# Kernel tuning notes

Measured on AMD Instinct MI355X. Metric: run time of the kernel, lower is better.

Reference implementation:

```python
import jax, jax.numpy as jnp
import numpy as np

EMBED = 2048
HEADS = 16
HEAD_DIM = EMBED // HEADS


def setup_inputs() -> dict:
    key = jax.random.key(0)
    k1, k2 = jax.random.split(key)
    X = jax.random.normal(k1, (2, 2048, EMBED), dtype=jnp.float32)
    W_qkv = jax.random.normal(k2, (EMBED, 3 * EMBED), dtype=jnp.float32) * (1.0 / np.sqrt(EMBED))
    b_qkv = jnp.zeros((3 * EMBED,), dtype=jnp.float32)
    return {"X": X, "W_qkv": W_qkv, "b_qkv": b_qkv}


def reference(X, W_qkv, b_qkv):
    B, S, D = X.shape
    qkv = jnp.einsum('bsd,de->bse', X, W_qkv) + b_qkv  # [B,S,3D]
    q, k, v = jnp.split(qkv, 3, axis=-1)
    # [B,S,D] -> [B,H,S,hd]
    def heads(t):
        return t.reshape(B, S, HEADS, HEAD_DIM).transpose(0, 2, 1, 3)
    q, k, v = heads(q), heads(k), heads(v)
    scale = 1.0 / np.sqrt(HEAD_DIM).astype(np.float32)
    attention_score = jnp.einsum('bhqd,bhkd->bhqk', q, k) * scale
    scores = jax.nn.softmax(attention_score, axis=-1)  # [B,H,S,S]
    attention = jnp.einsum('bhqk,bhkd->bhqd', scores, v)
    attention = attention.transpose(0, 2, 1, 3).reshape(B, S, D)
    return (attention, scores)
```

## Files before the change

### kernel.cpp

```cpp
#include <hip/hip_runtime.h>
#include <hip/hip_bf16.h>

typedef __attribute__((ext_vector_type(8))) short short8;
typedef __attribute__((ext_vector_type(4))) float floatx4;

#define SEQ 2048
#define EMB 2048
#define NH 16
#define HD 128
#define E3 6144

static __device__ __forceinline__ unsigned short f2bf(float f) {
  unsigned u = __builtin_bit_cast(unsigned, f);
  u += 0x7fffu + ((u >> 16) & 1u);
  return (unsigned short)(u >> 16);
}

__global__ void k_tw(const float* __restrict__ W, unsigned short* __restrict__ Wt) {
  __shared__ unsigned short t[32][33];
  int tx = threadIdx.x, ty = threadIdx.y;
  int e0 = blockIdx.x * 32, d0 = blockIdx.y * 32;
#pragma unroll
  for (int k = 0; k < 4; k++)
    t[ty + k * 8][tx] = f2bf(W[(long)(d0 + ty + k * 8) * E3 + e0 + tx]);
  __syncthreads();
#pragma unroll
  for (int k = 0; k < 4; k++)
    Wt[(long)(e0 + ty + k * 8) * EMB + d0 + tx] = t[tx][ty + k * 8];
}

__global__ void k_tv(const unsigned short* __restrict__ qkv, unsigned short* __restrict__ Vt) {
  __shared__ unsigned short t[32][33];
  int tx = threadIdx.x, ty = threadIdx.y;
  int z = blockIdx.z;
  int b = z >> 4, h = z & 15;
  int s0 = blockIdx.x * 32, d0 = blockIdx.y * 32;
#pragma unroll
  for (int k = 0; k < 4; k++) {
    int s = s0 + ty + k * 8;
    t[ty + k * 8][tx] = qkv[(long)(b * SEQ + s) * E3 + 2 * EMB + h * HD + d0 + tx];
  }
  __syncthreads();
#pragma unroll
  for (int k = 0; k < 4; k++) {
    int d = d0 + ty + k * 8;
    Vt[((long)z * HD + d) * SEQ + s0 + tx] = t[tx][ty + k * 8];
  }
}

template <int MODE>
__global__ __launch_bounds__(256, 2) void k_gemm(const void* __restrict__ Abase,
                                                 const unsigned short* __restrict__ Btb,
                                                 void* __restrict__ Cb,
                                                 const float* __restrict__ bias,
                                                 float scale) {
  constexpr int K = (MODE == 1) ? 128 : 2048;
  constexpr long sA = (MODE == 0) ? EMB : (MODE == 1) ? E3 : SEQ;
  constexpr long sB = (MODE == 0) ? EMB : (MODE == 1) ? E3 : SEQ;
  constexpr long sC = (MODE == 0) ? E3 : (MODE == 1) ? SEQ : EMB;
  constexpr bool AF32 = (MODE != 1);

  int z = blockIdx.z;
  long offA = 0, offB = 0, offC = 0;
  if (MODE == 1) {
    int b = z >> 4, h = z & 15;
    offA = (long)(b * SEQ) * E3 + h * HD;
    offB = (long)(b * SEQ) * E3 + EMB + h * HD;
    offC = (long)z * SEQ * SEQ;
  } else if (MODE == 2) {
    int b = z >> 4, h = z & 15;
    offA = (long)z * SEQ * SEQ;
    offB = (long)z * HD * SEQ;
    offC = (long)b * SEQ * EMB + h * HD;
  }

  __shared__ unsigned short As[128][72];
  __shared__ unsigned short Bs[128][72];

  int tid = threadIdx.x;
  int lane = tid & 63;
  int wave = tid >> 6;
  int wm = wave >> 1, wn = wave & 1;
  int quad = lane >> 4, l16 = lane & 15;
  long tM = (long)blockIdx.y * 128;
  long tN = (long)blockIdx.x * 128;

  const float* Af = (const float*)Abase;
  const unsigned short* Ab = (const unsigned short*)Abase;

  floatx4 acc[4][4] = {};

  for (int k0 = 0; k0 < K; k0 += 64) {
#pragma unroll
    for (int c = 0; c < 4; c++) {
      int id = tid + 256 * c;
      int r = id >> 3;
      int col = (id & 7) * 8;
      if (AF32) {
        const float* s = Af + offA + (tM + r) * sA + k0 + col;
        float4 f0 = *(const float4*)s;
        float4 f1 = *(const float4*)(s + 4);
        uint4 u;
        u.x = (unsigned)f2bf(f0.x) | ((unsigned)f2bf(f0.y) << 16);
        u.y = (unsigned)f2bf(f0.z) | ((unsigned)f2bf(f0.w) << 16);
        u.z = (unsigned)f2bf(f1.x) | ((unsigned)f2bf(f1.y) << 16);
        u.w = (unsigned)f2bf(f1.z) | ((unsigned)f2bf(f1.w) << 16);
        *(uint4*)&As[r][col] = u;
      } else {
        *(uint4*)&As[r][col] = *(const uint4*)(Ab + offA + (tM + r) * sA + k0 + col);
      }
      *(uint4*)&Bs[r][col] = *(const uint4*)(Btb + offB + (tN + r) * sB + k0 + col);
    }
    __syncthreads();
#pragma unroll
    for (int ks = 0; ks < 2; ks++) {
      short8 af[4], bfr[4];
#pragma unroll
      for (int i = 0; i < 4; i++)
        af[i] = *(const short8*)&As[wm * 64 + i * 16 + l16][ks * 32 + quad * 8];
#pragma unroll
      for (int j = 0; j < 4; j++)
        bfr[j] = *(const short8*)&Bs[wn * 64 + j * 16 + l16][ks * 32 + quad * 8];
#pragma unroll
      for (int i = 0; i < 4; i++)
#pragma unroll
        for (int j = 0; j < 4; j++)
          acc[i][j] = __builtin_amdgcn_mfma_f32_16x16x32_bf16(af[i], bfr[j], acc[i][j], 0, 0, 0);
    }
    __syncthreads();
  }

#pragma unroll
  for (int i = 0; i < 4; i++)
#pragma unroll
    for (int j = 0; j < 4; j++)
#pragma unroll
      for (int r = 0; r < 4; r++) {
        long row = tM + wm * 64 + i * 16 + quad * 4 + r;
        long col = tN + wn * 64 + j * 16 + l16;
        float v = acc[i][j][r];
        if (MODE == 0) {
          ((unsigned short*)Cb)[row * sC + col] = f2bf(v + bias[col]);
        } else if (MODE == 1) {
          ((float*)Cb)[offC + row * sC + col] = v * scale;
        } else {
          ((float*)Cb)[offC + row * sC + col] = v;
        }
      }
}

__global__ __launch_bounds__(256) void k_softmax(float* __restrict__ sc) {
  long row = blockIdx.x;
  float* p = sc + row * 2048;
  int t = threadIdx.x;
  int lane = t & 63, wave = t >> 6;
  float4 v0 = *(float4*)(p + t * 8);
  float4 v1 = *(float4*)(p + t * 8 + 4);
  float m = fmaxf(fmaxf(fmaxf(v0.x, v0.y), fmaxf(v0.z, v0.w)),
                  fmaxf(fmaxf(v1.x, v1.y), fmaxf(v1.z, v1.w)));
#pragma unroll
  for (int o = 32; o > 0; o >>= 1) m = fmaxf(m, __shfl_xor(m, o, 64));
  __shared__ float rm[4], rs[4];
  if (lane == 0) rm[wave] = m;
  __syncthreads();
  m = fmaxf(fmaxf(rm[0], rm[1]), fmaxf(rm[2], rm[3]));
  v0.x = __expf(v0.x - m); v0.y = __expf(v0.y - m);
  v0.z = __expf(v0.z - m); v0.w = __expf(v0.w - m);
  v1.x = __expf(v1.x - m); v1.y = __expf(v1.y - m);
  v1.z = __expf(v1.z - m); v1.w = __expf(v1.w - m);
  float s = v0.x + v0.y + v0.z + v0.w + v1.x + v1.y + v1.z + v1.w;
#pragma unroll
  for (int o = 32; o > 0; o >>= 1) s += __shfl_xor(s, o, 64);
  if (lane == 0) rs[wave] = s;
  __syncthreads();
  s = rs[0] + rs[1] + rs[2] + rs[3];
  float inv = 1.0f / s;
  v0.x *= inv; v0.y *= inv; v0.z *= inv; v0.w *= inv;
  v1.x *= inv; v1.y *= inv; v1.z *= inv; v1.w *= inv;
  *(float4*)(p + t * 8) = v0;
  *(float4*)(p + t * 8 + 4) = v1;
}

extern "C" void kernel_launch(void* const* d_in, const int* in_sizes, int n_in,
                              void* d_out, int out_size, void* d_ws, size_t ws_size,
                              hipStream_t stream) {
  const float* X = (const float*)d_in[0];
  const float* W = (const float*)d_in[1];
  const float* bias = (const float*)d_in[2];
  float* out = (float*)d_out;
  float* attn = out;
  float* scores = out + (long)2 * SEQ * EMB;

  unsigned short* Wt = (unsigned short*)d_ws;
  unsigned short* qkv = Wt + (long)E3 * EMB;
  unsigned short* Vt = qkv + (long)2 * SEQ * E3;

  k_tw<<<dim3(E3 / 32, EMB / 32), dim3(32, 8), 0, stream>>>(W, Wt);
  k_gemm<0><<<dim3(E3 / 128, (2 * SEQ) / 128, 1), 256, 0, stream>>>(X, Wt, qkv, bias, 1.0f);
  k_tv<<<dim3(SEQ / 32, HD / 32, 2 * NH), dim3(32, 8), 0, stream>>>(qkv, Vt);
  k_gemm<1><<<dim3(SEQ / 128, SEQ / 128, 2 * NH), 256, 0, stream>>>(qkv, qkv, scores, nullptr,
                                                                    0.08838834764831843f);
  k_softmax<<<dim3(2 * NH * SEQ), 256, 0, stream>>>(scores);
  k_gemm<2><<<dim3(1, SEQ / 128, 2 * NH), 256, 0, stream>>>(scores, Vt, attn, nullptr, 1.0f);
}
```

Measured before the change: 1.185 ms.

## Fuse QK^T, softmax and PV into a single two-pass attention kernel

Replaces the separate score GEMM, row softmax and PV GEMM with one kernel per (batch, head, 128-query tile). The first pass accumulates exp-scores into row sums and the P·V product on the fly. The second pass recomputes QK^T and writes the normalised fp32 scores once. This removes several full passes over the 512 MB fp32 score matrix, at the cost of doing the QK^T matmul twice. It also drops the max subtraction before exp, which is only safe while scores stay small.

```diff
diff --git a/kernel.cpp b/kernel.cpp
--- a/kernel.cpp
+++ b/kernel.cpp
@@ -9,6 +9,7 @@
 #define NH 16
 #define HD 128
 #define E3 6144
+#define SC2 0.12751224765383853f
 
 static __device__ __forceinline__ unsigned short f2bf(float f) {
   unsigned u = __builtin_bit_cast(unsigned, f);
@@ -149,36 +150,167 @@
       }
 }
 
-__global__ __launch_bounds__(256) void k_softmax(float* __restrict__ sc) {
-  long row = blockIdx.x;
-  float* p = sc + row * 2048;
-  int t = threadIdx.x;
-  int lane = t & 63, wave = t >> 6;
-  float4 v0 = *(float4*)(p + t * 8);
-  float4 v1 = *(float4*)(p + t * 8 + 4);
-  float m = fmaxf(fmaxf(fmaxf(v0.x, v0.y), fmaxf(v0.z, v0.w)),
-                  fmaxf(fmaxf(v1.x, v1.y), fmaxf(v1.z, v1.w)));
-#pragma unroll
-  for (int o = 32; o > 0; o >>= 1) m = fmaxf(m, __shfl_xor(m, o, 64));
-  __shared__ float rm[4], rs[4];
-  if (lane == 0) rm[wave] = m;
-  __syncthreads();
-  m = fmaxf(fmaxf(rm[0], rm[1]), fmaxf(rm[2], rm[3]));
-  v0.x = __expf(v0.x - m); v0.y = __expf(v0.y - m);
-  v0.z = __expf(v0.z - m); v0.w = __expf(v0.w - m);
-  v1.x = __expf(v1.x - m); v1.y = __expf(v1.y - m);
-  v1.z = __expf(v1.z - m); v1.w = __expf(v1.w - m);
-  float s = v0.x + v0.y + v0.z + v0.w + v1.x + v1.y + v1.z + v1.w;
-#pragma unroll
-  for (int o = 32; o > 0; o >>= 1) s += __shfl_xor(s, o, 64);
-  if (lane == 0) rs[wave] = s;
-  __syncthreads();
-  s = rs[0] + rs[1] + rs[2] + rs[3];
-  float inv = 1.0f / s;
-  v0.x *= inv; v0.y *= inv; v0.z *= inv; v0.w *= inv;
-  v1.x *= inv; v1.y *= inv; v1.z *= inv; v1.w *= inv;
-  *(float4*)(p + t * 8) = v0;
-  *(float4*)(p + t * 8 + 4) = v1;
+__global__ __launch_bounds__(256, 2) void k_attn(const unsigned short* __restrict__ qkv,
+                                                 const unsigned short* __restrict__ Vt,
+                                                 float* __restrict__ scores,
+                                                 float* __restrict__ attn) {
+  int id = blockIdx.x;
+  int z = (id & 7) * 4 + ((id >> 3) >> 4);
+  int qt = (id >> 3) & 15;
+  int b = z >> 4, h = z & 15;
+
+  const unsigned short* Qg = qkv + (long)b * SEQ * E3 + h * HD;
+  const unsigned short* Kg = Qg + EMB;
+  const unsigned short* Vg = Vt + (long)z * HD * SEQ;
+  float* Sg = scores + (long)z * SEQ * SEQ + (long)qt * 128 * SEQ;
+  float* Og = attn + (long)b * SEQ * EMB + (long)qt * 128 * EMB + h * HD;
+
+  __shared__ unsigned short Kt[64][136];
+  __shared__ unsigned short Vs[128][72];
+  __shared__ unsigned short Ps[128][72];
+
+  int tid = threadIdx.x;
+  int lane = tid & 63, wave = tid >> 6;
+  int quad = lane >> 4, l16 = lane & 15;
+
+  short8 qf[2][4];
+#pragma unroll
+  for (int i = 0; i < 2; i++)
+#pragma unroll
+    for (int ks = 0; ks < 4; ks++)
+      qf[i][ks] = *(const short8*)(Qg + (long)(qt * 128 + wave * 32 + i * 16 + l16) * E3 +
+                                   ks * 32 + quad * 8);
+
+  floatx4 oacc[2][8] = {};
+  float rs[2][4] = {};
+
+  uint4 kreg[4], vreg[4];
+  auto loadK = [&](int t) {
+#pragma unroll
+    for (int c = 0; c < 4; c++) {
+      int i2 = tid + 256 * c;
+      kreg[c] = *(const uint4*)(Kg + (long)(t * 64 + (i2 >> 4)) * E3 + (i2 & 15) * 8);
+    }
+  };
+  auto loadV = [&](int t) {
+#pragma unroll
+    for (int c = 0; c < 4; c++) {
+      int i2 = tid + 256 * c;
+      vreg[c] = *(const uint4*)(Vg + (long)(i2 >> 3) * SEQ + t * 64 + (i2 & 7) * 8);
+    }
+  };
+
+  loadK(0);
+  loadV(0);
+
+  for (int t = 0; t < 32; t++) {
+#pragma unroll
+    for (int c = 0; c < 4; c++) {
+      int i2 = tid + 256 * c;
+      *(uint4*)&Kt[i2 >> 4][(i2 & 15) * 8] = kreg[c];
+      *(uint4*)&Vs[i2 >> 3][(i2 & 7) * 8] = vreg[c];
+    }
+    __syncthreads();
+    if (t < 31) { loadK(t + 1); loadV(t + 1); }
+
+    floatx4 sacc[2][4] = {};
+#pragma unroll
+    for (int ks = 0; ks < 4; ks++) {
+      short8 kf[4];
+#pragma unroll
+      for (int j = 0; j < 4; j++)
+        kf[j] = *(const short8*)&Kt[j * 16 + l16][ks * 32 + quad * 8];
+#pragma unroll
+      for (int i = 0; i < 2; i++)
+#pragma unroll
+        for (int j = 0; j < 4; j++)
+          sacc[i][j] = __builtin_amdgcn_mfma_f32_16x16x32_bf16(qf[i][ks], kf[j], sacc[i][j], 0, 0, 0);
+    }
+#pragma unroll
+    for (int i = 0; i < 2; i++)
+#pragma unroll
+      for (int j = 0; j < 4; j++)
+#pragma unroll
+        for (int r = 0; r < 4; r++) {
+          float e = exp2f(sacc[i][j][r] * SC2);
+          rs[i][r] += e;
+          Ps[wave * 32 + i * 16 + quad * 4 + r][j * 16 + l16] = f2bf(e);
+        }
+    __syncthreads();
+#pragma unroll
+    for (int ks = 0; ks < 2; ks++) {
+      short8 pf[2], vf[8];
+#pragma unroll
+      for (int i = 0; i < 2; i++)
+        pf[i] = *(const short8*)&Ps[wave * 32 + i * 16 + l16][ks * 32 + quad * 8];
+#pragma unroll
+      for (int j = 0; j < 8; j++)
+        vf[j] = *(const short8*)&Vs[j * 16 + l16][ks * 32 + quad * 8];
+#pragma unroll
+      for (int i = 0; i < 2; i++)
+#pragma unroll
+        for (int j = 0; j < 8; j++)
+          oacc[i][j] = __builtin_amdgcn_mfma_f32_16x16x32_bf16(pf[i], vf[j], oacc[i][j], 0, 0, 0);
+    }
+    __syncthreads();
+  }
+
+  loadK(0);
+
+  float irs[2][4];
+#pragma unroll
+  for (int i = 0; i < 2; i++)
+#pragma unroll
+    for (int r = 0; r < 4; r++) {
+      float s = rs[i][r];
+      s += __shfl_xor(s, 1, 64);
+      s += __shfl_xor(s, 2, 64);
+      s += __shfl_xor(s, 4, 64);
+      s += __shfl_xor(s, 8, 64);
+      irs[i][r] = 1.0f / s;
+    }
+
+#pragma unroll
+  for (int i = 0; i < 2; i++)
+#pragma unroll
+    for (int j = 0; j < 8; j++)
+#pragma unroll
+      for (int r = 0; r < 4; r++)
+        Og[(long)(wave * 32 + i * 16 + quad * 4 + r) * EMB + j * 16 + l16] =
+            oacc[i][j][r] * irs[i][r];
+
+  for (int t = 0; t < 32; t++) {
+#pragma unroll
+    for (int c = 0; c < 4; c++) {
+      int i2 = tid + 256 * c;
+      *(uint4*)&Kt[i2 >> 4][(i2 & 15) * 8] = kreg[c];
+    }
+    __syncthreads();
+    if (t < 31) loadK(t + 1);
+
+    floatx4 sacc[2][4] = {};
+#pragma unroll
+    for (int ks = 0; ks < 4; ks++) {
+      short8 kf[4];
+#pragma unroll
+      for (int j = 0; j < 4; j++)
+        kf[j] = *(const short8*)&Kt[j * 16 + l16][ks * 32 + quad * 8];
+#pragma unroll
+      for (int i = 0; i < 2; i++)
+#pragma unroll
+        for (int j = 0; j < 4; j++)
+          sacc[i][j] = __builtin_amdgcn_mfma_f32_16x16x32_bf16(qf[i][ks], kf[j], sacc[i][j], 0, 0, 0);
+    }
+#pragma unroll
+    for (int i = 0; i < 2; i++)
+#pragma unroll
+      for (int j = 0; j < 4; j++)
+#pragma unroll
+        for (int r = 0; r < 4; r++)
+          Sg[(long)(wave * 32 + i * 16 + quad * 4 + r) * SEQ + t * 64 + j * 16 + l16] =
+              exp2f(sacc[i][j][r] * SC2) * irs[i][r];
+    __syncthreads();
+  }
 }
 
 extern "C" void kernel_launch(void* const* d_in, const int* in_sizes, int n_in,
@@ -198,8 +330,5 @@
   k_tw<<<dim3(E3 / 32, EMB / 32), dim3(32, 8), 0, stream>>>(W, Wt);
   k_gemm<0><<<dim3(E3 / 128, (2 * SEQ) / 128, 1), 256, 0, stream>>>(X, Wt, qkv, bias, 1.0f);
   k_tv<<<dim3(SEQ / 32, HD / 32, 2 * NH), dim3(32, 8), 0, stream>>>(qkv, Vt);
-  k_gemm<1><<<dim3(SEQ / 128, SEQ / 128, 2 * NH), 256, 0, stream>>>(qkv, qkv, scores, nullptr,
-                                                                    0.08838834764831843f);
-  k_softmax<<<dim3(2 * NH * SEQ), 256, 0, stream>>>(scores);
-  k_gemm<2><<<dim3(1, SEQ / 128, 2 * NH), 256, 0, stream>>>(scores, Vt, attn, nullptr, 1.0f);
-}
+  k_attn<<<dim3(512), dim3(256), 0, stream>>>(qkv, Vt, scores, attn);
+}
```

New measurement: 1.161 ms. 2.0% less time.
